# Kernel optimization log

Hardware: AMD Instinct MI355X
Metric: run time of the kernel (lower is better)

The kernel has to match this reference:

```python
import jax, jax.numpy as jnp
import numpy as np

N = 10000      # atoms
E = 160000     # edges (avg degree 16)
H = 64         # hidden_channels
R = 64         # num_rbf
MAXZ = 100
RC = 4.5       # cutoff_upper (cutoff_lower = 0)
LN_EPS = 1e-5


def setup_inputs() -> dict:
    key = jax.random.key(0)
    ks = jax.random.split(key, 20)
    z = jax.random.randint(ks[0], (N,), 0, MAXZ, dtype=jnp.int32)
    edge_index = jax.random.randint(ks[1], (2, E), 0, N, dtype=jnp.int32)
    edge_weight = jax.random.uniform(ks[2], (E,), dtype=jnp.float32) * RC
    v = jax.random.normal(ks[3], (E, 3), dtype=jnp.float32)
    edge_vec_norm = v / jnp.linalg.norm(v, axis=-1, keepdims=True)
    edge_attr = jax.random.normal(ks[4], (E, R), dtype=jnp.float32)
    p = lambda k, shape: (jax.random.normal(k, shape, dtype=jnp.float32) * 0.1)
    return {
        'z': z, 'edge_index': edge_index, 'edge_weight': edge_weight,
        'edge_vec_norm': edge_vec_norm, 'edge_attr': edge_attr,
        'emb': p(ks[5], (MAXZ, H)),
        'emb2_w': p(ks[6], (H, 2 * H)), 'emb2_b': p(ks[7], (H,)),
        'dp1_w': p(ks[8], (H, R)), 'dp1_b': p(ks[9], (H,)),
        'dp2_w': p(ks[10], (H, R)), 'dp2_b': p(ks[11], (H,)),
        'dp3_w': p(ks[12], (H, R)), 'dp3_b': p(ks[13], (H,)),
        'ln_g': jnp.ones((H,), jnp.float32), 'ln_b': jnp.zeros((H,), jnp.float32),
        'w1': p(ks[14], (2 * H, H)), 'b1': jnp.zeros((2 * H,), jnp.float32),
        'w2': p(ks[15], (3 * H, 2 * H)), 'b2': jnp.zeros((3 * H,), jnp.float32),
        'm0': p(ks[16], (H, H)), 'm1': p(ks[17], (H, H)), 'm2': p(ks[18], (H, H)),
    }


def reference(z, edge_index, edge_weight, edge_vec_norm, edge_attr,
              emb, emb2_w, emb2_b, dp1_w, dp1_b, dp2_w, dp2_b, dp3_w, dp3_b,
              ln_g, ln_b, w1, b1, w2, b2, m0, m1, m2):
    n_atoms = z.shape[0]
    hc = emb.shape[1]
    src, dst = edge_index[0], edge_index[1]

    # atomic number message Z_ij: concat(Z_i, Z_j) -> Linear  [E,H]
    Zn = emb[z]
    Zij = jnp.concatenate([Zn[src], Zn[dst]], axis=-1) @ emb2_w.T + emb2_b

    # cosine cutoff (cutoff_lower == 0)
    C = 0.5 * (jnp.cos(edge_weight * jnp.pi / RC) + 1.0) * (edge_weight < RC)

    # RBF-gated per-edge channel weights, all [E,H]
    g1 = (edge_attr @ dp1_w.T + dp1_b) * C[:, None] * Zij
    g2 = (edge_attr @ dp2_w.T + dp2_b) * C[:, None] * Zij
    g3 = (edge_attr @ dp3_w.T + dp3_b) * C[:, None] * Zij

    eye = jnp.eye(3, dtype=Zij.dtype)
    vx, vy, vz = edge_vec_norm[:, 0], edge_vec_norm[:, 1], edge_vec_norm[:, 2]
    zero = jnp.zeros_like(vx)
    skew = jnp.stack([zero, -vz, vy, vz, zero, -vx, -vy, vx, zero], axis=-1).reshape(-1, 3, 3)
    outer = edge_vec_norm[:, :, None] * edge_vec_norm[:, None, :]  # [E,3,3], symmetric
    sym = outer - (jnp.trace(outer, axis1=-2, axis2=-1) / 3.0)[:, None, None] * eye

    # per-edge messages [E,H,3,3]
    Iij = g1[:, :, None, None] * eye
    Aij = g2[:, :, None, None] * skew[:, None, :, :]
    Sij = g3[:, :, None, None] * sym[:, None, :, :]

    # scatter-add to atoms
    I = jax.ops.segment_sum(Iij, src, num_segments=n_atoms)
    A = jax.ops.segment_sum(Aij, src, num_segments=n_atoms)
    S = jax.ops.segment_sum(Sij, src, num_segments=n_atoms)

    # tensor norm -> layernorm -> MLP1
    tn = ((I + A + S) ** 2).sum((-2, -1))  # [N,H]
    mu = tn.mean(-1, keepdims=True)
    var = ((tn - mu) ** 2).mean(-1, keepdims=True)
    norm = (tn - mu) / jnp.sqrt(var + LN_EPS) * ln_g + ln_b
    norm = jax.nn.silu(norm @ w1.T + b1)
    norm = jax.nn.silu(norm @ w2.T + b2)
    norm = norm.reshape(-1, hc, 3)
    n0 = norm[..., 0][:, :, None, None]

    # channel-mixing; NOTE: original code applies MLP2[1]/MLP2[2] to the
    # updated I and gates all three with norm[...,0] -- replicated faithfully.
    I = jnp.einsum('nhij,kh->nkij', I, m0) * n0
    A = jnp.einsum('nhij,kh->nkij', I, m1) * n0
    S = jnp.einsum('nhij,kh->nkij', I, m2) * n0
    return I + A + S
```

## Files before the change

kernel.cpp:

```cpp
#include <hip/hip_runtime.h>
#include <stdint.h>

#define NATOMS 10000
#define NEDGES 160000
#define RCUT   4.5f
#define CAP    64

#define T_BYTES    ((size_t)NATOMS * 640 * 4)
#define CNT_OFF    (T_BYTES)
#define CNT_BYTES  ((size_t)NATOMS * 4)
#define REC_OFF    (CNT_OFF + CNT_BYTES)
#define REC_BYTES  ((size_t)NATOMS * CAP * 16)
#define EMB_OFF    (REC_OFF + REC_BYTES)
#define EMB_BYTES  ((size_t)100 * 64 * 2)

typedef unsigned short u16;
typedef __bf16 bf16x8 __attribute__((ext_vector_type(8)));
typedef float  f32x4  __attribute__((ext_vector_type(4)));

#define MFMA16(a,b,c) __builtin_amdgcn_mfma_f32_16x16x32_bf16((a),(b),(c),0,0,0)
#define BFMAGIC 0x3F803F80u
#define MSK 0xffff0000u

__device__ __forceinline__ float uf(unsigned int u){ return __uint_as_float(u); }
__device__ __forceinline__ float b2f(u16 u){
  union { unsigned int i; float f; } v; v.i = ((unsigned int)u) << 16; return v.f;
}
__device__ __forceinline__ u16 f2b(float f){
  union { unsigned int i; float f; } v; v.f = f;
  unsigned int b = v.i + 0x7fffu + ((v.i >> 16) & 1u);
  return (u16)(b >> 16);
}
__device__ __forceinline__ float ldf(const void* p, int i, int bf){
  if (bf) return b2f(((const u16*)p)[i]);
  return ((const float*)p)[i];
}
__device__ __forceinline__ bf16x8 ld8bf(const void* p, int i, int bf){
  if (bf) return *(const bf16x8*)((const u16*)p + i);
  const float4* q = (const float4*)((const float*)p + i);
  float4 a = q[0], b = q[1];
  bf16x8 r;
  r[0]=(__bf16)a.x; r[1]=(__bf16)a.y; r[2]=(__bf16)a.z; r[3]=(__bf16)a.w;
  r[4]=(__bf16)b.x; r[5]=(__bf16)b.y; r[6]=(__bf16)b.z; r[7]=(__bf16)b.w;
  return r;
}
__device__ __forceinline__ uint4 ld8pk(const void* p, int i, int bf){
  if (bf) return *(const uint4*)((const u16*)p + i);
  const float4* q = (const float4*)((const float*)p + i);
  float4 a = q[0], b = q[1];
  uint4 r;
  r.x = (unsigned int)f2b(a.x) | ((unsigned int)f2b(a.y) << 16);
  r.y = (unsigned int)f2b(a.z) | ((unsigned int)f2b(a.w) << 16);
  r.z = (unsigned int)f2b(b.x) | ((unsigned int)f2b(b.y) << 16);
  r.w = (unsigned int)f2b(b.z) | ((unsigned int)f2b(b.w) << 16);
  return r;
}
__device__ __forceinline__ void ld8f(const void* p, int i, float* o, int bf){
  if (bf){
    uint4 v = *(const uint4*)((const u16*)p + i);
    o[0]=uf(v.x<<16); o[1]=uf(v.x&MSK); o[2]=uf(v.y<<16); o[3]=uf(v.y&MSK);
    o[4]=uf(v.z<<16); o[5]=uf(v.z&MSK); o[6]=uf(v.w<<16); o[7]=uf(v.w&MSK);
    return;
  }
  const float4* q = (const float4*)((const float*)p + i);
  float4 a = q[0], b = q[1];
  o[0]=a.x; o[1]=a.y; o[2]=a.z; o[3]=a.w; o[4]=b.x; o[5]=b.y; o[6]=b.z; o[7]=b.w;
}
__device__ __forceinline__ uint4 pk8(const float* f){
  uint4 r;
  r.x = (unsigned int)f2b(f[0]) | ((unsigned int)f2b(f[1]) << 16);
  r.y = (unsigned int)f2b(f[2]) | ((unsigned int)f2b(f[3]) << 16);
  r.z = (unsigned int)f2b(f[4]) | ((unsigned int)f2b(f[5]) << 16);
  r.w = (unsigned int)f2b(f[6]) | ((unsigned int)f2b(f[7]) << 16);
  return r;
}

__global__ __launch_bounds__(256) void scatter_kernel(const int* __restrict__ ei,
                                                      const int* __restrict__ z,
                                                      const void* __restrict__ ew,
                                                      const void* __restrict__ evn,
                                                      const void* __restrict__ emb,
                                                      u16* __restrict__ emb16,
                                                      int* __restrict__ cnt,
                                                      uint4* __restrict__ REC,
                                                      const unsigned int* __restrict__ lng){
  const int bf = (lng[0] == BFMAGIC);
  int e = blockIdx.x * 256 + threadIdx.x;
  if (e < 6400) emb16[e] = bf ? ((const u16*)emb)[e] : f2b(((const float*)emb)[e]);
  int s = ei[e], d = ei[NEDGES + e];
  int p = atomicAdd(&cnt[s], 1);
  const float w  = ldf(ew, e, bf);
  const float Cv = (w < RCUT) ? 0.5f*(__cosf(w * (3.14159265358979f / RCUT)) + 1.0f) : 0.0f;
  uint4 rec;
  rec.x = (unsigned int)e;
  rec.y = (unsigned int)z[d];
  rec.z = (unsigned int)f2b(ldf(evn, 3*e + 0, bf)) | ((unsigned int)f2b(ldf(evn, 3*e + 1, bf)) << 16);
  rec.w = (unsigned int)f2b(ldf(evn, 3*e + 2, bf)) | ((unsigned int)f2b(Cv) << 16);
  if (p < CAP) REC[(size_t)s*CAP + p] = rec;
}

__global__ __launch_bounds__(256) void atomT_kernel(
    const int* __restrict__ z,
    const u16* __restrict__ emb16,
    const void* __restrict__ attr,
    const uint4* __restrict__ REC,
    const int* __restrict__ cnt,
    const void* __restrict__ e2w, const void* __restrict__ e2b,
    const void* __restrict__ d1w, const void* __restrict__ d1b,
    const void* __restrict__ d2w, const void* __restrict__ d2b,
    const void* __restrict__ d3w, const void* __restrict__ d3b,
    float* __restrict__ T,
    const unsigned int* __restrict__ lng)
{
  __shared__ __align__(16) u16 dpW[3][64][64];
  __shared__ __align__(16) u16 e2W[64][128];

  const int bf  = (lng[0] == BFMAGIC);
  const int tid = threadIdx.x;
  const void* dps[3] = {d1w, d2w, d3w};
  for (int idx = tid; idx < 1536; idx += 256){
    int w = idx >> 9, rem = idx & 511, r = rem >> 3, c8 = rem & 7;
    *(bf16x8*)&dpW[w][r][(c8 ^ (r & 7))*8] = ld8bf(dps[w], r*64 + c8*8, bf);
  }
  for (int idx = tid; idx < 1024; idx += 256){
    int r = idx >> 4, c8 = idx & 15;
    *(bf16x8*)&e2W[r][(c8 ^ (r & 7))*8] = ld8bf(e2w, r*128 + c8*8, bf);
  }
  __syncthreads();

  const int lane = tid & 63;
  const int wave = tid >> 6;
  const int hh   = lane & 15;
  const int quad = lane >> 4;
  const int half = wave & 1;
  const int ntb  = half * 2;

  float be2[2], bd1[2], bd2[2], bd3[2];
#pragma unroll
  for (int j = 0; j < 2; j++){
    int h = hh + 16*(ntb + j);
    be2[j] = ldf(e2b, h, bf); bd1[j] = ldf(d1b, h, bf);
    bd2[j] = ldf(d2b, h, bf); bd3[j] = ldf(d3b, h, bf);
  }

  const int n  = blockIdx.x * 2 + (wave >> 1);
  const int e0 = n * CAP;
  const int e1 = e0 + min(cnt[n], CAP);
  const int zs = z[n];
  bf16x8 zf0 = *(const bf16x8*)(emb16 + zs*64 + quad*8);
  bf16x8 zf1 = *(const bf16x8*)(emb16 + zs*64 + 32 + quad*8);

  float P[10][2];
#pragma unroll
  for (int c = 0; c < 10; c++){ P[c][0] = 0.f; P[c][1] = 0.f; }

  for (int base = e0; base < e1; base += 16){
    const int iiA = min(base + hh, e1 - 1);
    const uint4 recA = REC[iiA];
    bf16x8 af0 = ld8bf(attr, (int)recA.x*64 + quad*8, bf);
    bf16x8 af1 = ld8bf(attr, (int)recA.x*64 + 32 + quad*8, bf);
    bf16x8 zf2 = *(const bf16x8*)(emb16 + recA.y*64 + quad*8);
    bf16x8 zf3 = *(const bf16x8*)(emb16 + recA.y*64 + 32 + quad*8);

    f32x4 aZ[2], a1[2], a2[2], a3[2];
#pragma unroll
    for (int j = 0; j < 2; j++){
      aZ[j] = (f32x4){0.f,0.f,0.f,0.f};
      a1[j] = (f32x4){0.f,0.f,0.f,0.f};
      a2[j] = (f32x4){0.f,0.f,0.f,0.f};
      a3[j] = (f32x4){0.f,0.f,0.f,0.f};
    }

#pragma unroll
    for (int j = 0; j < 2; j++){
      const int h  = hh + 16*(ntb + j);
      const int s0 = (quad       ^ (h & 7)) * 8;
      const int s1 = ((quad + 4) ^ (h & 7)) * 8;
      bf16x8 b;
      b = *(const bf16x8*)&dpW[0][h][s0];           a1[j] = MFMA16(af0, b, a1[j]);
      b = *(const bf16x8*)&dpW[0][h][s1];           a1[j] = MFMA16(af1, b, a1[j]);
      b = *(const bf16x8*)&dpW[1][h][s0];           a2[j] = MFMA16(af0, b, a2[j]);
      b = *(const bf16x8*)&dpW[1][h][s1];           a2[j] = MFMA16(af1, b, a2[j]);
      b = *(const bf16x8*)&dpW[2][h][s0];           a3[j] = MFMA16(af0, b, a3[j]);
      b = *(const bf16x8*)&dpW[2][h][s1];           a3[j] = MFMA16(af1, b, a3[j]);
      b = *(const bf16x8*)&e2W[h][s0];              aZ[j] = MFMA16(zf0, b, aZ[j]);
      b = *(const bf16x8*)&e2W[h][s1];              aZ[j] = MFMA16(zf1, b, aZ[j]);
      b = *(const bf16x8*)&e2W[h][((quad + 8)  ^ (h & 7)) * 8];  aZ[j] = MFMA16(zf2, b, aZ[j]);
      b = *(const bf16x8*)&e2W[h][((quad + 12) ^ (h & 7)) * 8];  aZ[j] = MFMA16(zf3, b, aZ[j]);
    }

#pragma unroll
    for (int r = 0; r < 4; r++){
      const int ii = base + quad*4 + r;
      const bool ea = (ii < e1);
      const uint4 rec = REC[ea ? ii : (e1 - 1)];
      const float Cv = ea ? b2f((u16)(rec.w >> 16)) : 0.f;
      const float vx = b2f((u16)(rec.z & 0xffffu));
      const float vy = b2f((u16)(rec.z >> 16));
      const float vz = b2f((u16)(rec.w & 0xffffu));
      const float xx = vx*vx - (1.f/3.f), yy = vy*vy - (1.f/3.f), zz = vz*vz - (1.f/3.f);
      const float xy = vx*vy, xz = vx*vz, yz = vy*vz;
#pragma unroll
      for (int j = 0; j < 2; j++){
        const float czv = Cv * (aZ[j][r] + be2[j]);
        const float g1 = (a1[j][r] + bd1[j]) * czv;
        const float g2 = (a2[j][r] + bd2[j]) * czv;
        const float g3 = (a3[j][r] + bd3[j]) * czv;
        P[0][j] += g1;
        P[1][j] += g2*vx; P[2][j] += g2*vy; P[3][j] += g2*vz;
        P[4][j] += g3*xx; P[5][j] += g3*yy; P[6][j] += g3*zz;
        P[7][j] += g3*xy; P[8][j] += g3*xz; P[9][j] += g3*yz;
      }
    }
  }

#pragma unroll
  for (int c = 0; c < 10; c++)
#pragma unroll
    for (int j = 0; j < 2; j++){
      float v = P[c][j];
      v += __shfl_xor(v, 16, 64);
      v += __shfl_xor(v, 32, 64);
      P[c][j] = v;
    }

  if ((quad >> 1) == half){
    float* Tn = T + (size_t)n * 640;
#pragma unroll
    for (int c = 0; c < 10; c++)
      Tn[c*64 + lane] = P[c][quad & 1];
  }
}

__global__ __launch_bounds__(256) void mlp_kernel(
    const float* __restrict__ T,
    const void* __restrict__ ln_g, const void* __restrict__ ln_b,
    const void* __restrict__ w1,  const void* __restrict__ b1,
    const void* __restrict__ w2,  const void* __restrict__ b2p,
    const void* __restrict__ m0,  const void* __restrict__ m1,
    const void* __restrict__ m2,  void* __restrict__ out,
    const unsigned int* __restrict__ lng)
{
  __shared__ __align__(16) u16 w1L[128][72];
  __shared__ __align__(16) u16 w2L[64][136];
  __shared__ __align__(16) u16 m0L[64][72];
  __shared__ __align__(16) u16 msL[64][72];
  __shared__ __align__(16) float xbuf[4][64];
  __shared__ __align__(16) float hbuf2[4][128];
  __shared__ __align__(16) float isoB[4][64];
  __shared__ __align__(16) float i1B[4][64];

  const int bf  = (lng[0] == BFMAGIC);
  const int tid = threadIdx.x;

  for (int idx = tid; idx < 1024; idx += 256){
    int r = idx >> 3, c8 = idx & 7;
    *(uint4*)&w1L[r][c8*8] = ld8pk(w1, r*64 + c8*8, bf);
  }
  for (int idx = tid; idx < 1024; idx += 256){
    int r = idx >> 4, c8 = idx & 15;
    *(uint4*)&w2L[r][c8*8] = ld8pk(w2, (3*r)*128 + c8*8, bf);
  }
  for (int idx = tid; idx < 512; idx += 256){
    int r = idx >> 3, c8 = idx & 7;
    *(uint4*)&m0L[r][c8*8] = ld8pk(m0, r*64 + c8*8, bf);
    float f[8], g[8];
    ld8f(m1, r*64 + c8*8, f, bf);
    ld8f(m2, r*64 + c8*8, g, bf);
#pragma unroll
    for (int q = 0; q < 8; q++) f[q] += g[q];
    *(uint4*)&msL[r][c8*8] = pk8(f);
  }
  __syncthreads();

  const int wave = tid >> 6;
  const int h    = tid & 63;
  const int wid  = blockIdx.x * 4 + wave;

  const float lngh = ldf(ln_g, h, bf), lnbh = ldf(ln_b, h, bf);
  const float b1a = ldf(b1, h, bf), b1b = ldf(b1, h + 64, bf);
  const float b2h = ldf(b2p, 3*h, bf);

  const uint4*  A4 = (const uint4*)&w1L[h][0];
  const uint4*  B4 = (const uint4*)&w1L[h + 64][0];
  const uint4*  W4 = (const uint4*)&w2L[h][0];
  const uint4*  M4 = (const uint4*)&m0L[h][0];
  const uint4*  S4 = (const uint4*)&msL[h][0];
  const float4* X4  = (const float4*)&xbuf[wave][0];
  const float4* H4  = (const float4*)&hbuf2[wave][0];
  const float4* I4  = (const float4*)&isoB[wave][0];
  const float4* J4  = (const float4*)&i1B[wave][0];

  const int NITER = (NATOMS + 2047) / 2048;
  for (int it = 0; it < NITER; it++){
    const int n   = wid + it * 2048;
    const bool act = (n < NATOMS);
    const int na  = act ? n : 0;

    const float* Tn = T + (size_t)na * 640;
    const float iso = Tn[h];
    const float wx = Tn[64+h], wy = Tn[128+h], wz = Tn[192+h];
    const float sxx = Tn[256+h], syy = Tn[320+h], szz = Tn[384+h];
    const float sxy = Tn[448+h], sxz = Tn[512+h], syz = Tn[576+h];
    const float tn = (iso+sxx)*(iso+sxx) + (iso+syy)*(iso+syy) + (iso+szz)*(iso+szz)
                   + 2.f*(sxy*sxy + sxz*sxz + syz*syz + wx*wx + wy*wy + wz*wz);
    isoB[wave][h] = iso;

    float s = tn;
#pragma unroll
    for (int off = 32; off; off >>= 1) s += __shfl_xor(s, off, 64);
    const float mu = s * (1.f/64.f);
    const float d0 = tn - mu;
    float v = d0 * d0;
#pragma unroll
    for (int off = 32; off; off >>= 1) v += __shfl_xor(v, off, 64);
    v *= (1.f/64.f);
    xbuf[wave][h] = d0 * rsqrtf(v + 1e-5f) * lngh + lnbh;
    __syncthreads();

    float acc0 = b1a, acc1 = b1b;
#pragma unroll
    for (int q = 0; q < 8; q++){
      const uint4 A = A4[q], B = B4[q];
      const float4 x0 = X4[2*q], x1 = X4[2*q + 1];
      acc0 += uf(A.x << 16)*x0.x + uf(A.x & MSK)*x0.y;
      acc0 += uf(A.y << 16)*x0.z + uf(A.y & MSK)*x0.w;
      acc0 += uf(A.z << 16)*x1.x + uf(A.z & MSK)*x1.y;
      acc0 += uf(A.w << 16)*x1.z + uf(A.w & MSK)*x1.w;
      acc1 += uf(B.x << 16)*x0.x + uf(B.x & MSK)*x0.y;
      acc1 += uf(B.y << 16)*x0.z + uf(B.y & MSK)*x0.w;
      acc1 += uf(B.z << 16)*x1.x + uf(B.z & MSK)*x1.y;
      acc1 += uf(B.w << 16)*x1.z + uf(B.w & MSK)*x1.w;
    }
    acc0 = acc0 / (1.f + __expf(-acc0));
    acc1 = acc1 / (1.f + __expf(-acc1));
    hbuf2[wave][h] = acc0; hbuf2[wave][h + 64] = acc1;
    __syncthreads();

    float acc2 = b2h, t1 = 0.f;
#pragma unroll
    for (int q = 0; q < 16; q++){
      const uint4 W = W4[q];
      const float4 y0 = H4[2*q], y1 = H4[2*q + 1];
      acc2 += uf(W.x << 16)*y0.x + uf(W.x & MSK)*y0.y;
      acc2 += uf(W.y << 16)*y0.z + uf(W.y & MSK)*y0.w;
      acc2 += uf(W.z << 16)*y1.x + uf(W.z & MSK)*y1.y;
      acc2 += uf(W.w << 16)*y1.z + uf(W.w & MSK)*y1.w;
    }
#pragma unroll
    for (int q = 0; q < 8; q++){
      const uint4 M = M4[q];
      const float4 x0 = I4[2*q], x1 = I4[2*q + 1];
      t1 += uf(M.x << 16)*x0.x + uf(M.x & MSK)*x0.y;
      t1 += uf(M.y << 16)*x0.z + uf(M.y & MSK)*x0.w;
      t1 += uf(M.z << 16)*x1.x + uf(M.z & MSK)*x1.y;
      t1 += uf(M.w << 16)*x1.z + uf(M.w & MSK)*x1.w;
    }
    const float n0 = acc2 / (1.f + __expf(-acc2));
    const float iso1 = t1 * n0;
    i1B[wave][h] = iso1;
    __syncthreads();

    float t23 = 0.f;
#pragma unroll
    for (int q = 0; q < 8; q++){
      const uint4 M = S4[q];
      const float4 x0 = J4[2*q], x1 = J4[2*q + 1];
      t23 += uf(M.x << 16)*x0.x + uf(M.x & MSK)*x0.y;
      t23 += uf(M.y << 16)*x0.z + uf(M.y & MSK)*x0.w;
      t23 += uf(M.z << 16)*x1.x + uf(M.z & MSK)*x1.y;
      t23 += uf(M.w << 16)*x1.z + uf(M.w & MSK)*x1.w;
    }
    const float dval = iso1 + t23 * n0;

    if (act){
      if (bf){
        u16* o = (u16*)out + (size_t)n * 576 + h * 9;
        const u16 db = f2b(dval);
        o[0] = db; o[1] = 0; o[2] = 0;
        o[3] = 0;  o[4] = db; o[5] = 0;
        o[6] = 0;  o[7] = 0;  o[8] = db;
      } else {
        float* o = (float*)out + (size_t)n * 576 + h * 9;
        o[0] = dval; o[1] = 0.f; o[2] = 0.f;
        o[3] = 0.f;  o[4] = dval; o[5] = 0.f;
        o[6] = 0.f;  o[7] = 0.f;  o[8] = dval;
      }
    }
    __syncthreads();
  }
}

extern "C" void kernel_launch(void* const* d_in, const int* in_sizes, int n_in,
                              void* d_out, int out_size, void* d_ws, size_t ws_size,
                              hipStream_t stream) {
  const int* z    = (const int*)d_in[0];
  const int* ei   = (const int*)d_in[1];
  const void* ew   = d_in[2];
  const void* evn  = d_in[3];
  const void* attr = d_in[4];
  const void* emb  = d_in[5];
  const void* e2w  = d_in[6];
  const void* e2b  = d_in[7];
  const void* d1w  = d_in[8];
  const void* d1b  = d_in[9];
  const void* d2w  = d_in[10];
  const void* d2b  = d_in[11];
  const void* d3w  = d_in[12];
  const void* d3b  = d_in[13];
  const void* ln_g = d_in[14];
  const void* ln_b = d_in[15];
  const void* w1   = d_in[16];
  const void* b1   = d_in[17];
  const void* w2   = d_in[18];
  const void* b2p  = d_in[19];
  const void* m0   = d_in[20];
  const void* m1   = d_in[21];
  const void* m2   = d_in[22];
  const unsigned int* lng = (const unsigned int*)ln_g;

  char* ws = (char*)d_ws;
  float*   T     = (float*)ws;
  int*     cnt   = (int*)(ws + CNT_OFF);
  uint4*   REC   = (uint4*)(ws + REC_OFF);
  u16*     emb16 = (u16*)(ws + EMB_OFF);

  hipMemsetAsync(cnt, 0, CNT_BYTES, stream);
  scatter_kernel<<<NEDGES/256, 256, 0, stream>>>(ei, z, ew, evn, emb, emb16, cnt, REC, lng);
  atomT_kernel<<<NATOMS/2, 256, 0, stream>>>(z, emb16, attr, REC, cnt, e2w, e2b,
                                             d1w, d1b, d2w, d2b, d3w, d3b, T, lng);
  mlp_kernel<<<512, 256, 0, stream>>>(T, ln_g, ln_b, w1, b1, w2, b2p,
                                      m0, m1, m2, d_out, lng);
}
```

Baseline: 270.1 us.

## Make atomT kernel persistent with prefetched edge records and shuffle-based record reuse

The per-atom tensor kernel becomes a persistent grid of 1024 blocks that loop over atom pairs, so the shared-memory weight staging is paid once per block instead of once per atom pair. The next chunk's edge record and the next atom's count and species are loaded ahead of use. The second per-edge record load in the epilogue is replaced by lane shuffles of the already-loaded record. Occupancy hint launch_bounds(256,4) is added. The cost is possible register pressure and less latency hiding from the smaller grid.

After: 366.7 us. 1.36x slower.

```diff
diff --git a/kernel.cpp b/kernel.cpp
--- a/kernel.cpp
+++ b/kernel.cpp
@@ -5,6 +5,7 @@
 #define NEDGES 160000
 #define RCUT   4.5f
 #define CAP    64
+#define ATGRID 1024
 
 #define T_BYTES    ((size_t)NATOMS * 640 * 4)
 #define CNT_OFF    (T_BYTES)
@@ -99,7 +100,7 @@
   if (p < CAP) REC[(size_t)s*CAP + p] = rec;
 }
 
-__global__ __launch_bounds__(256) void atomT_kernel(
+__global__ __launch_bounds__(256, 4) void atomT_kernel(
     const int* __restrict__ z,
     const u16* __restrict__ emb16,
     const void* __restrict__ attr,
@@ -134,6 +135,7 @@
   const int quad = lane >> 4;
   const int half = wave & 1;
   const int ntb  = half * 2;
+  const int wpair = wave >> 1;
 
   float be2[2], bd1[2], bd2[2], bd3[2];
 #pragma unroll
@@ -143,92 +145,112 @@
     bd2[j] = ldf(d2b, h, bf); bd3[j] = ldf(d3b, h, bf);
   }
 
-  const int n  = blockIdx.x * 2 + (wave >> 1);
-  const int e0 = n * CAP;
-  const int e1 = e0 + min(cnt[n], CAP);
-  const int zs = z[n];
-  bf16x8 zf0 = *(const bf16x8*)(emb16 + zs*64 + quad*8);
-  bf16x8 zf1 = *(const bf16x8*)(emb16 + zs*64 + 32 + quad*8);
-
-  float P[10][2];
-#pragma unroll
-  for (int c = 0; c < 10; c++){ P[c][0] = 0.f; P[c][1] = 0.f; }
-
-  for (int base = e0; base < e1; base += 16){
-    const int iiA = min(base + hh, e1 - 1);
-    const uint4 recA = REC[iiA];
-    bf16x8 af0 = ld8bf(attr, (int)recA.x*64 + quad*8, bf);
-    bf16x8 af1 = ld8bf(attr, (int)recA.x*64 + 32 + quad*8, bf);
-    bf16x8 zf2 = *(const bf16x8*)(emb16 + recA.y*64 + quad*8);
-    bf16x8 zf3 = *(const bf16x8*)(emb16 + recA.y*64 + 32 + quad*8);
-
-    f32x4 aZ[2], a1[2], a2[2], a3[2];
-#pragma unroll
-    for (int j = 0; j < 2; j++){
-      aZ[j] = (f32x4){0.f,0.f,0.f,0.f};
-      a1[j] = (f32x4){0.f,0.f,0.f,0.f};
-      a2[j] = (f32x4){0.f,0.f,0.f,0.f};
-      a3[j] = (f32x4){0.f,0.f,0.f,0.f};
-    }
-
-#pragma unroll
-    for (int j = 0; j < 2; j++){
-      const int h  = hh + 16*(ntb + j);
-      const int s0 = (quad       ^ (h & 7)) * 8;
-      const int s1 = ((quad + 4) ^ (h & 7)) * 8;
-      bf16x8 b;
-      b = *(const bf16x8*)&dpW[0][h][s0];           a1[j] = MFMA16(af0, b, a1[j]);
-      b = *(const bf16x8*)&dpW[0][h][s1];           a1[j] = MFMA16(af1, b, a1[j]);
-      b = *(const bf16x8*)&dpW[1][h][s0];           a2[j] = MFMA16(af0, b, a2[j]);
-      b = *(const bf16x8*)&dpW[1][h][s1];           a2[j] = MFMA16(af1, b, a2[j]);
-      b = *(const bf16x8*)&dpW[2][h][s0];           a3[j] = MFMA16(af0, b, a3[j]);
-      b = *(const bf16x8*)&dpW[2][h][s1];           a3[j] = MFMA16(af1, b, a3[j]);
-      b = *(const bf16x8*)&e2W[h][s0];              aZ[j] = MFMA16(zf0, b, aZ[j]);
-      b = *(const bf16x8*)&e2W[h][s1];              aZ[j] = MFMA16(zf1, b, aZ[j]);
-      b = *(const bf16x8*)&e2W[h][((quad + 8)  ^ (h & 7)) * 8];  aZ[j] = MFMA16(zf2, b, aZ[j]);
-      b = *(const bf16x8*)&e2W[h][((quad + 12) ^ (h & 7)) * 8];  aZ[j] = MFMA16(zf3, b, aZ[j]);
-    }
-
-#pragma unroll
-    for (int r = 0; r < 4; r++){
-      const int ii = base + quad*4 + r;
-      const bool ea = (ii < e1);
-      const uint4 rec = REC[ea ? ii : (e1 - 1)];
-      const float Cv = ea ? b2f((u16)(rec.w >> 16)) : 0.f;
-      const float vx = b2f((u16)(rec.z & 0xffffu));
-      const float vy = b2f((u16)(rec.z >> 16));
-      const float vz = b2f((u16)(rec.w & 0xffffu));
-      const float xx = vx*vx - (1.f/3.f), yy = vy*vy - (1.f/3.f), zz = vz*vz - (1.f/3.f);
-      const float xy = vx*vy, xz = vx*vz, yz = vy*vz;
+  int pr  = blockIdx.x;
+  int n   = pr * 2 + wpair;
+  int cn  = cnt[n];
+  int zsv = z[n];
+
+  while (true) {
+    const int e0   = n * CAP;
+    const int nv   = min(cn, CAP);
+    const int e1   = e0 + nv;
+    const int e1m1 = (nv > 0) ? (e1 - 1) : e0;
+    uint4 recA = REC[min(e0 + hh, e1m1)];
+
+    bf16x8 zf0 = *(const bf16x8*)(emb16 + zsv*64 + quad*8);
+    bf16x8 zf1 = *(const bf16x8*)(emb16 + zsv*64 + 32 + quad*8);
+
+    const int prn  = pr + ATGRID;
+    const bool more = (prn < NATOMS/2);
+    const int nn   = prn * 2 + wpair;
+    if (more){ cn = cnt[nn]; zsv = z[nn]; }
+
+    float P[10][2];
+#pragma unroll
+    for (int c = 0; c < 10; c++){ P[c][0] = 0.f; P[c][1] = 0.f; }
+
+    for (int base = e0; base < e1; base += 16){
+      uint4 recN = REC[min(base + 16 + hh, e1m1)];
+
+      bf16x8 af0 = ld8bf(attr, (int)recA.x*64 + quad*8, bf);
+      bf16x8 af1 = ld8bf(attr, (int)recA.x*64 + 32 + quad*8, bf);
+      bf16x8 zf2 = *(const bf16x8*)(emb16 + recA.y*64 + quad*8);
+      bf16x8 zf3 = *(const bf16x8*)(emb16 + recA.y*64 + 32 + quad*8);
+
+      f32x4 aZ[2], a1[2], a2[2], a3[2];
 #pragma unroll
       for (int j = 0; j < 2; j++){
-        const float czv = Cv * (aZ[j][r] + be2[j]);
-        const float g1 = (a1[j][r] + bd1[j]) * czv;
-        const float g2 = (a2[j][r] + bd2[j]) * czv;
-        const float g3 = (a3[j][r] + bd3[j]) * czv;
-        P[0][j] += g1;
-        P[1][j] += g2*vx; P[2][j] += g2*vy; P[3][j] += g2*vz;
-        P[4][j] += g3*xx; P[5][j] += g3*yy; P[6][j] += g3*zz;
-        P[7][j] += g3*xy; P[8][j] += g3*xz; P[9][j] += g3*yz;
+        aZ[j] = (f32x4){0.f,0.f,0.f,0.f};
+        a1[j] = (f32x4){0.f,0.f,0.f,0.f};
+        a2[j] = (f32x4){0.f,0.f,0.f,0.f};
+        a3[j] = (f32x4){0.f,0.f,0.f,0.f};
       }
-    }
-  }
-
-#pragma unroll
-  for (int c = 0; c < 10; c++)
-#pragma unroll
-    for (int j = 0; j < 2; j++){
-      float v = P[c][j];
-      v += __shfl_xor(v, 16, 64);
-      v += __shfl_xor(v, 32, 64);
-      P[c][j] = v;
-    }
-
-  if ((quad >> 1) == half){
-    float* Tn = T + (size_t)n * 640;
+
+#pragma unroll
+      for (int j = 0; j < 2; j++){
+        const int h  = hh + 16*(ntb + j);
+        const int s0 = (quad       ^ (h & 7)) * 8;
+        const int s1 = ((quad + 4) ^ (h & 7)) * 8;
+        bf16x8 b;
+        b = *(const bf16x8*)&dpW[0][h][s0];           a1[j] = MFMA16(af0, b, a1[j]);
+        b = *(const bf16x8*)&dpW[0][h][s1];           a1[j] = MFMA16(af1, b, a1[j]);
+        b = *(const bf16x8*)&dpW[1][h][s0];           a2[j] = MFMA16(af0, b, a2[j]);
+        b = *(const bf16x8*)&dpW[1][h][s1];           a2[j] = MFMA16(af1, b, a2[j]);
+        b = *(const bf16x8*)&dpW[2][h][s0];           a3[j] = MFMA16(af0, b, a3[j]);
+        b = *(const bf16x8*)&dpW[2][h][s1];           a3[j] = MFMA16(af1, b, a3[j]);
+        b = *(const bf16x8*)&e2W[h][s0];              aZ[j] = MFMA16(zf0, b, aZ[j]);
+        b = *(const bf16x8*)&e2W[h][s1];              aZ[j] = MFMA16(zf1, b, aZ[j]);
+        b = *(const bf16x8*)&e2W[h][((quad + 8)  ^ (h & 7)) * 8];  aZ[j] = MFMA16(zf2, b, aZ[j]);
+        b = *(const bf16x8*)&e2W[h][((quad + 12) ^ (h & 7)) * 8];  aZ[j] = MFMA16(zf3, b, aZ[j]);
+      }
+
+#pragma unroll
+      for (int r = 0; r < 4; r++){
+        const int ii = base + quad*4 + r;
+        const bool ea = (ii < e1);
+        const int srcl = quad*20 + r;
+        const unsigned int rz = (unsigned int)__shfl((int)recA.z, srcl, 64);
+        const unsigned int rw = (unsigned int)__shfl((int)recA.w, srcl, 64);
+        const float Cv = ea ? b2f((u16)(rw >> 16)) : 0.f;
+        const float vx = b2f((u16)(rz & 0xffffu));
+        const float vy = b2f((u16)(rz >> 16));
+        const float vz = b2f((u16)(rw & 0xffffu));
+        const float xx = vx*vx - (1.f/3.f), yy = vy*vy - (1.f/3.f), zz = vz*vz - (1.f/3.f);
+        const float xy = vx*vy, xz = vx*vz, yz = vy*vz;
+#pragma unroll
+        for (int j = 0; j < 2; j++){
+          const float czv = Cv * (aZ[j][r] + be2[j]);
+          const float g1 = (a1[j][r] + bd1[j]) * czv;
+          const float g2 = (a2[j][r] + bd2[j]) * czv;
+          const float g3 = (a3[j][r] + bd3[j]) * czv;
+          P[0][j] += g1;
+          P[1][j] += g2*vx; P[2][j] += g2*vy; P[3][j] += g2*vz;
+          P[4][j] += g3*xx; P[5][j] += g3*yy; P[6][j] += g3*zz;
+          P[7][j] += g3*xy; P[8][j] += g3*xz; P[9][j] += g3*yz;
+        }
+      }
+      recA = recN;
+    }
+
 #pragma unroll
     for (int c = 0; c < 10; c++)
-      Tn[c*64 + lane] = P[c][quad & 1];
+#pragma unroll
+      for (int j = 0; j < 2; j++){
+        float v = P[c][j];
+        v += __shfl_xor(v, 16, 64);
+        v += __shfl_xor(v, 32, 64);
+        P[c][j] = v;
+      }
+
+    if ((quad >> 1) == half){
+      float* Tn = T + (size_t)n * 640;
+#pragma unroll
+      for (int c = 0; c < 10; c++)
+        Tn[c*64 + lane] = P[c][quad & 1];
+    }
+
+    if (!more) break;
+    pr = prn; n = nn;
   }
 }
 
@@ -427,8 +449,8 @@
 
   hipMemsetAsync(cnt, 0, CNT_BYTES, stream);
   scatter_kernel<<<NEDGES/256, 256, 0, stream>>>(ei, z, ew, evn, emb, emb16, cnt, REC, lng);
-  atomT_kernel<<<NATOMS/2, 256, 0, stream>>>(z, emb16, attr, REC, cnt, e2w, e2b,
-                                             d1w, d1b, d2w, d2b, d3w, d3b, T, lng);
+  atomT_kernel<<<ATGRID, 256, 0, stream>>>(z, emb16, attr, REC, cnt, e2w, e2b,
+                                           d1w, d1b, d2w, d2b, d3w, d3b, T, lng);
   mlp_kernel<<<512, 256, 0, stream>>>(T, ln_g, ln_b, w1, b1, w2, b2p,
                                       m0, m1, m2, d_out, lng);
 }
```
